# Optimization experiments

Measured on AMD Instinct MI355X. Metric: run time of the kernel, lower is better.

## Reference

```python
import jax, jax.numpy as jnp
import numpy as np

N = 50000      # nodes
E = 800000     # edges (avg degree 16)
IN_DIM = 64
EMB = 64
L = 4          # num_layer
BN_EPS = 1e-5


def setup_inputs() -> dict:
    key = jax.random.key(0)
    ks = jax.random.split(key, 8)
    s = 0.05
    return {
        "x": jax.random.normal(ks[0], (N, 1, IN_DIM), jnp.float32),
        "edge_index": jax.random.randint(ks[1], (2, E), 0, N, jnp.int32),
        "edge_attr": jax.random.normal(ks[2], (E, 3), jnp.float32),
        "edge_weight": jax.random.uniform(ks[3], (E,), jnp.float32),
        # atom encoder Linear(in_dim, emb)
        "ae_w": jax.random.normal(ks[4], (IN_DIM, EMB), jnp.float32) * s,
        "ae_b": jnp.zeros((EMB,), jnp.float32),
        # per-layer GIN MLP: Linear -> BN -> ReLU -> Linear (stacked over L)
        "W1": jax.random.normal(ks[5], (L, EMB, EMB), jnp.float32) * s,
        "b1": jnp.zeros((L, EMB), jnp.float32),
        "g1": jnp.ones((L, EMB), jnp.float32),
        "be1": jnp.zeros((L, EMB), jnp.float32),
        "W2": jax.random.normal(ks[6], (L, EMB, EMB), jnp.float32) * s,
        "b2": jnp.zeros((L, EMB), jnp.float32),
        # outer per-layer BatchNorm1d in GNN_node
        "g_out": jnp.ones((L, EMB), jnp.float32),
        "be_out": jnp.zeros((L, EMB), jnp.float32),
    }


def _bn(h, g, b):
    # BatchNorm1d, training mode: batch stats over node dim, biased variance
    m = h.mean(0)
    v = h.var(0)
    return (h - m) * jax.lax.rsqrt(v + BN_EPS) * g + b


def reference(x, edge_index, edge_attr, edge_weight,
              ae_w, ae_b, W1, b1, g1, be1, W2, b2, g_out, be_out):
    # atom encoder on x[:, 0] : [N, in_dim] -> [N, emb]
    h = x[:, 0] @ ae_w + ae_b
    src = edge_index[0]
    dst = edge_index[1]
    n = h.shape[0]
    num_layers = W1.shape[0]
    for l in range(num_layers):
        # MyPyGINConv (train_eps=False, eps=0): scatter-add of x_j * w_e, plus self term
        msg = h[src] * edge_weight[:, None]                      # [E, emb]
        agg = jax.ops.segment_sum(msg, dst, num_segments=n)      # [N, emb]
        out = agg + h                                            # (1+eps)*x_r, eps=0
        # conv MLP: Linear -> BN -> ReLU -> Linear
        out = jax.nn.relu(_bn(out @ W1[l] + b1[l], g1[l], be1[l]))
        out = out @ W2[l] + b2[l]
        # outer BN + ReLU (always applied for 'originalgin'); dropout p=0; residual
        out = jax.nn.relu(_bn(out, g_out[l], be_out[l]))
        h = out + h
    return h  # JK='last'
```

## Files before the change

### kernel.cpp

```cpp
#include <hip/hip_runtime.h>
#include <stdint.h>

#define EMB 64
#define BN_EPS 1e-5f
#define BSH 8
#define CHUNK 4096
#define TS 68
#define NHB 120

typedef short bfrag __attribute__((ext_vector_type(8)));
typedef float f32x4 __attribute__((ext_vector_type(4)));

#define IN_F32    0
#define IN_BF16   1
#define IN_BF16BN 2

__device__ __forceinline__ unsigned short f2b(float x) {
    unsigned u = __float_as_uint(x);
    u += 0x7FFFu + ((u >> 16) & 1u);
    return (unsigned short)(u >> 16);
}
__device__ __forceinline__ float b2f(unsigned short v) {
    return __uint_as_float(((unsigned)v) << 16);
}

__global__ void __launch_bounds__(256) k_prep_hist(
        const float* __restrict__ ae_w, const float* __restrict__ W1,
        const float* __restrict__ W2, unsigned short* __restrict__ Wt16,
        int* __restrict__ hist_part, float* __restrict__ stats,
        const int* __restrict__ ei, int E, int L, int nstats) {
    __shared__ int lh[256];
    const int tid = threadIdx.x;
    const int nw = (1 + 2 * L) * EMB * EMB;
    for (int gid = blockIdx.x * 256 + tid; gid < nw; gid += gridDim.x * 256) {
        int m = gid >> 12;
        int j = (gid >> 6) & 63;
        int k = gid & 63;
        const float* src = (m == 0) ? ae_w
                         : (m <= L ? W1 + (size_t)(m - 1) * EMB * EMB
                                   : W2 + (size_t)(m - 1 - L) * EMB * EMB);
        Wt16[gid] = f2b(src[k * EMB + j]);
    }
    for (int i = blockIdx.x * 256 + tid; i < nstats; i += gridDim.x * 256)
        stats[i] = 0.0f;
    if (blockIdx.x < NHB) {
        lh[tid] = 0;
        __syncthreads();
        for (int e = blockIdx.x * 256 + tid; e < E; e += NHB * 256)
            atomicAdd(&lh[((unsigned)ei[E + e]) >> BSH], 1);
        __syncthreads();
        hist_part[blockIdx.x * 256 + tid] = lh[tid];
    }
}

__global__ void __launch_bounds__(256) k_bscan(const int* __restrict__ hist_part,
                                               int* __restrict__ bbase,
                                               int* __restrict__ bcur, int nb) {
    __shared__ int a[256];
    const int t = threadIdx.x;
    int v = 0;
    for (int b = 0; b < NHB; b++) v += hist_part[b * 256 + t];
    a[t] = v;
    __syncthreads();
    for (int off = 1; off < 256; off <<= 1) {
        int x = (t >= off) ? a[t - off] : 0;
        __syncthreads();
        a[t] += x;
        __syncthreads();
    }
    int excl = a[t] - v;
    if (t < nb) { bbase[t] = excl; bcur[t] = excl; }
    if (t == nb - 1) bbase[nb] = a[t];
}

__global__ void __launch_bounds__(256) k_part(
        const int* __restrict__ ei, const float* __restrict__ ew,
        int* __restrict__ bcur, int2* __restrict__ eG, int E) {
    __shared__ int lcnt[256], lbase[256], loff[256];
    const int tid = threadIdx.x;
    const int c0 = blockIdx.x * CHUNK;
    lcnt[tid] = 0;
    __syncthreads();
    int src[16], pk[16], g[16];
    float wt[16];
#pragma unroll
    for (int i = 0; i < 16; i++) {
        int e = c0 + i * 256 + tid;
        if (e < E) {
            int d = ei[E + e];
            src[i] = ei[e];
            wt[i] = ew[e];
            g[i] = ((unsigned)d) >> BSH;
            pk[i] = src[i] | ((d & 255) << 24);
            atomicAdd(&lcnt[g[i]], 1);
        } else g[i] = -1;
    }
    __syncthreads();
    if (lcnt[tid]) lbase[tid] = atomicAdd(&bcur[tid], lcnt[tid]);
    loff[tid] = 0;
    __syncthreads();
#pragma unroll
    for (int i = 0; i < 16; i++) {
        if (g[i] >= 0) {
            int pos = lbase[g[i]] + atomicAdd(&loff[g[i]], 1);
            eG[pos] = make_int2(pk[i], __float_as_int(wt[i]));
        }
    }
}

__global__ void __launch_bounds__(256) k_build(
        const int2* __restrict__ eG, const int* __restrict__ bbase,
        int* __restrict__ rowst, int* __restrict__ counts,
        int2* __restrict__ pairs, int N) {
    __shared__ int lcnt[256], a[256], lcur[256];
    const int t = threadIdx.x;
    const int b = blockIdx.x;
    const int e0 = bbase[b], e1 = bbase[b + 1];
    lcnt[t] = 0;
    __syncthreads();
    for (int i = e0 + t; i < e1; i += 256)
        atomicAdd(&lcnt[((unsigned)eG[i].x) >> 24], 1);
    __syncthreads();
    int v = lcnt[t];
    a[t] = v;
    __syncthreads();
    for (int off = 1; off < 256; off <<= 1) {
        int x = (t >= off) ? a[t - off] : 0;
        __syncthreads();
        a[t] += x;
        __syncthreads();
    }
    int excl = a[t] - v;
    lcur[t] = excl;
    int node = (b << BSH) + t;
    if (node < N) { rowst[node] = e0 + excl; counts[node] = v; }
    __syncthreads();
    for (int i = e0 + t; i < e1; i += 256) {
        int2 p = eG[i];
        int loc = ((unsigned)p.x) >> 24;
        int pos = e0 + atomicAdd(&lcur[loc], 1);
        pairs[pos] = make_int2(p.x & 0x00FFFFFF, p.y);
    }
}

__global__ void k_agg(const unsigned short* __restrict__ hb,
                      const int* __restrict__ rowst,
                      const int* __restrict__ counts, const int2* __restrict__ pairs,
                      unsigned short* __restrict__ out16, int N) {
    const int lane = threadIdx.x & 63;
    int wave = (blockIdx.x * blockDim.x + threadIdx.x) >> 6;
    const int nwaves = (gridDim.x * blockDim.x) >> 6;
    for (int nA = wave; nA < N; nA += 2 * nwaves) {
        const int nB = nA + nwaves;
        const int uA = __builtin_amdgcn_readfirstlane(nA);
        const int uB = __builtin_amdgcn_readfirstlane(nB);
        const bool hasB = uB < N;
        int sA = rowst[uA], eA = sA + counts[uA];
        int sB = 0, eB = 0;
        if (hasB) { sB = rowst[uB]; eB = sB + counts[uB]; }
        float aA[8] = {0, 0, 0, 0, 0, 0, 0, 0};
        float aB[8] = {0, 0, 0, 0, 0, 0, 0, 0};
        for (int xA = sA, xB = sB; (xA < eA) | (xB < eB); xA += 8, xB += 8) {
            int2 pA[8], pB[8];
            float wA[8], wB[8];
#pragma unroll
            for (int k = 0; k < 8; k++) {
                int i = xA + k;
                bool ok = i < eA;
                int2 p = pairs[ok ? i : 0];
                pA[k] = p;
                wA[k] = ok ? __int_as_float(p.y) : 0.f;
            }
#pragma unroll
            for (int k = 0; k < 8; k++) {
                int i = xB + k;
                bool ok = i < eB;
                int2 p = pairs[ok ? i : 0];
                pB[k] = p;
                wB[k] = ok ? __int_as_float(p.y) : 0.f;
            }
#pragma unroll
            for (int k = 0; k < 8; k++)
                aA[k] = fmaf(wA[k], b2f(hb[(size_t)pA[k].x * EMB + lane]), aA[k]);
#pragma unroll
            for (int k = 0; k < 8; k++)
                aB[k] = fmaf(wB[k], b2f(hb[(size_t)pB[k].x * EMB + lane]), aB[k]);
        }
        float sumA = (((aA[0] + aA[1]) + (aA[2] + aA[3])) +
                      ((aA[4] + aA[5]) + (aA[6] + aA[7]))) +
                     b2f(hb[(size_t)uA * EMB + lane]);
        out16[(size_t)uA * EMB + lane] = f2b(sumA);
        if (hasB) {
            float sumB = (((aB[0] + aB[1]) + (aB[2] + aB[3])) +
                          ((aB[4] + aB[5]) + (aB[6] + aB[7]))) +
                         b2f(hb[(size_t)uB * EMB + lane]);
            out16[(size_t)uB * EMB + lane] = f2b(sumB);
        }
    }
}

template <int INMODE, bool DO_STATS>
__global__ void __launch_bounds__(256) k_mmx(
        const void* __restrict__ in_v, const unsigned short* __restrict__ Wt,
        const float* __restrict__ bias, const float* __restrict__ stats,
        const float* __restrict__ g, const float* __restrict__ be, float invN,
        unsigned short* __restrict__ out16, float* __restrict__ st_out, int N) {
    __shared__ float tb[64 * TS];
    __shared__ float st_part[128];
    __shared__ float scs[EMB], shs[EMB];
    const int tid = threadIdx.x;
    const int lane = tid & 63;
    const int wv = tid >> 6;
    const int node0 = blockIdx.x * 64;
    const int m = lane & 15;
    const int quad = lane >> 4;

    if (DO_STATS && tid < 128) st_part[tid] = 0.f;
    if (INMODE == IN_BF16BN) {
        if (tid < EMB) {
            float s1 = 0.f, s2 = 0.f;
#pragma unroll
            for (int k = 0; k < 8; k++) {
                s1 += stats[k * 128 + tid];
                s2 += stats[k * 128 + 64 + tid];
            }
            float mm = s1 * invN;
            float va = fmaf(s2, invN, -mm * mm);
            float rs = rsqrtf(va + BN_EPS);
            float sc = rs * g[tid];
            scs[tid] = sc;
            shs[tid] = fmaf(-mm, sc, be[tid]);
        }
        __syncthreads();
    }

    const int arow = node0 + wv * 16 + m;
    bfrag a0 = {0, 0, 0, 0, 0, 0, 0, 0}, a1 = {0, 0, 0, 0, 0, 0, 0, 0};
    if (arow < N) {
        if (INMODE == IN_BF16) {
            const unsigned short* ab =
                (const unsigned short*)in_v + (size_t)arow * EMB + quad * 8;
            a0 = *(const bfrag*)ab;
            a1 = *(const bfrag*)(ab + 32);
        } else if (INMODE == IN_BF16BN) {
            const unsigned short* ab =
                (const unsigned short*)in_v + (size_t)arow * EMB + quad * 8;
            bfrag r0 = *(const bfrag*)ab;
            bfrag r1 = *(const bfrag*)(ab + 32);
#pragma unroll
            for (int j = 0; j < 8; j++) {
                int k0 = quad * 8 + j;
                float v0 = b2f((unsigned short)r0[j]);
                float v1 = b2f((unsigned short)r1[j]);
                v0 = fmaxf(0.f, fmaf(v0, scs[k0], shs[k0]));
                v1 = fmaxf(0.f, fmaf(v1, scs[k0 + 32], shs[k0 + 32]));
                a0[j] = (short)f2b(v0);
                a1[j] = (short)f2b(v1);
            }
        } else {
            const float* af = (const float*)in_v + (size_t)arow * EMB + quad * 8;
#pragma unroll
            for (int j = 0; j < 8; j++) {
                a0[j] = (short)f2b(af[j]);
                a1[j] = (short)f2b(af[32 + j]);
            }
        }
    }

    const unsigned short* bb = Wt + (size_t)m * EMB + quad * 8;
    f32x4 acc[4];
#pragma unroll
    for (int c = 0; c < 4; c++) {
        bfrag b0 = *(const bfrag*)(bb + c * 16 * EMB);
        bfrag b1 = *(const bfrag*)(bb + c * 16 * EMB + 32);
        f32x4 z = {0.f, 0.f, 0.f, 0.f};
        z = __builtin_amdgcn_mfma_f32_16x16x32_bf16(a0, b0, z, 0, 0, 0);
        z = __builtin_amdgcn_mfma_f32_16x16x32_bf16(a1, b1, z, 0, 0, 0);
        acc[c] = z;
    }

#pragma unroll
    for (int c = 0; c < 4; c++) {
        float bj = bias[c * 16 + m];
#pragma unroll
        for (int r = 0; r < 4; r++) {
            int row = wv * 16 + quad * 4 + r;
            float v = (node0 + row < N) ? (acc[c][r] + bj) : 0.f;
            tb[row * TS + c * 16 + m] = v;
        }
    }
    __syncthreads();

    if (DO_STATS) {
        float ssum = 0.f, ssq = 0.f;
#pragma unroll
        for (int i = 0; i < 16; i++) {
            float v = tb[(wv * 16 + i) * TS + lane];
            ssum += v;
            ssq = fmaf(v, v, ssq);
        }
        atomicAdd(&st_part[lane], ssum);
        atomicAdd(&st_part[64 + lane], ssq);
    }

    ushort4* o4 = (ushort4*)(out16 + (size_t)node0 * EMB);
#pragma unroll
    for (int it = 0; it < 4; it++) {
        int flat4 = it * 256 + tid;
        int nsub = flat4 >> 4;
        int c4 = flat4 & 15;
        if (node0 + nsub < N) {
            const float* s4 = tb + nsub * TS + c4 * 4;
            ushort4 o;
            o.x = f2b(s4[0]); o.y = f2b(s4[1]);
            o.z = f2b(s4[2]); o.w = f2b(s4[3]);
            o4[flat4] = o;
        }
    }

    if (DO_STATS) {
        __syncthreads();
        if (tid < 128)
            atomicAdd(&st_out[((unsigned)blockIdx.x & 7u) * 128 + tid], st_part[tid]);
    }
}

template <bool LAST>
__global__ void k_bnres(const unsigned short* __restrict__ u16,
                        const float* __restrict__ st,
                        const float* __restrict__ g, const float* __restrict__ be,
                        unsigned short* __restrict__ hb16, float* __restrict__ out32,
                        float invN, int total4) {
    __shared__ float scs[EMB], shs[EMB];
    const int tid = threadIdx.x;
    if (tid < EMB) {
        float s1 = 0.f, s2 = 0.f;
#pragma unroll
        for (int k = 0; k < 8; k++) {
            s1 += st[k * 128 + tid];
            s2 += st[k * 128 + 64 + tid];
        }
        float mm = s1 * invN;
        float va = fmaf(s2, invN, -mm * mm);
        float rs = rsqrtf(va + BN_EPS);
        float sc = rs * g[tid];
        scs[tid] = sc;
        shs[tid] = fmaf(-mm, sc, be[tid]);
    }
    __syncthreads();
    int stride = gridDim.x * blockDim.x;
    for (int i4 = blockIdx.x * blockDim.x + tid; i4 < total4; i4 += stride) {
        int c4 = i4 & 15;
        ushort4 uv = ((const ushort4*)u16)[i4];
        ushort4 hv = ((const ushort4*)hb16)[i4];
        float4 scv = *(const float4*)&scs[c4 * 4];
        float4 shv = *(const float4*)&shs[c4 * 4];
        float4 o;
        o.x = fmaxf(0.f, fmaf(b2f(uv.x), scv.x, shv.x)) + b2f(hv.x);
        o.y = fmaxf(0.f, fmaf(b2f(uv.y), scv.y, shv.y)) + b2f(hv.y);
        o.z = fmaxf(0.f, fmaf(b2f(uv.z), scv.z, shv.z)) + b2f(hv.z);
        o.w = fmaxf(0.f, fmaf(b2f(uv.w), scv.w, shv.w)) + b2f(hv.w);
        if (LAST) {
            ((float4*)out32)[i4] = o;
        } else {
            ushort4 ob;
            ob.x = f2b(o.x); ob.y = f2b(o.y);
            ob.z = f2b(o.z); ob.w = f2b(o.w);
            ((ushort4*)hb16)[i4] = ob;
        }
    }
}

extern "C" void kernel_launch(void* const* d_in, const int* in_sizes, int n_in,
                              void* d_out, int out_size, void* d_ws, size_t ws_size,
                              hipStream_t stream) {
    const float* x     = (const float*)d_in[0];
    const int*   ei    = (const int*)d_in[1];
    const float* ew    = (const float*)d_in[3];
    const float* ae_w  = (const float*)d_in[4];
    const float* ae_b  = (const float*)d_in[5];
    const float* W1    = (const float*)d_in[6];
    const float* b1    = (const float*)d_in[7];
    const float* g1    = (const float*)d_in[8];
    const float* be1   = (const float*)d_in[9];
    const float* W2    = (const float*)d_in[10];
    const float* b2    = (const float*)d_in[11];
    const float* g_out = (const float*)d_in[12];
    const float* be_out= (const float*)d_in[13];

    const int N = in_sizes[0] / EMB;
    const int E = in_sizes[3];
    const int L = in_sizes[6] / (EMB * EMB);
    const float invN = 1.0f / (float)N;
    const int NBUCK = (N + 255) >> BSH;

    uintptr_t p = (uintptr_t)d_ws;
    auto alloc = [&](size_t bytes) -> void* {
        p = (p + 255) & ~(uintptr_t)255;
        void* r = (void*)p;
        p += bytes;
        return r;
    };
    unsigned short* hb16 = (unsigned short*)alloc((size_t)N * EMB * 2);
    unsigned short* b16a = (unsigned short*)alloc((size_t)N * EMB * 2);
    unsigned short* t16  = (unsigned short*)alloc((size_t)N * EMB * 2);
    unsigned short* Wt16 = (unsigned short*)alloc((size_t)(1 + 2 * L) * EMB * EMB * 2);
    int*   counts= (int*)alloc((size_t)N * 4);
    int*   rowst = (int*)alloc((size_t)N * 4);
    int*   hist_part = (int*)alloc((size_t)NHB * 256 * 4);
    int*   bbase = (int*)alloc(257 * 4);
    int*   bcur  = (int*)alloc(256 * 4);
    int2*  pairs = (int2*)alloc((size_t)E * 8);
    int2*  eG    = (int2*)alloc((size_t)E * 8);
    float* stats = (float*)alloc((size_t)L * 2 * 8 * 128 * 4);
    (void)ws_size; (void)n_in; (void)out_size;

    const int nw = (1 + 2 * L) * EMB * EMB;
    const int nstats = L * 2 * 8 * 128;
    const int nprep = (nw + 255) / 256;
    hipLaunchKernelGGL(k_prep_hist, dim3(nprep > NHB ? nprep : NHB), dim3(256), 0,
                       stream, ae_w, W1, W2, Wt16, hist_part, stats, ei, E, L, nstats);

    const int ntiles = (N + 63) / 64;
    hipLaunchKernelGGL((k_mmx<IN_F32, false>), dim3(ntiles), dim3(256), 0, stream,
                       x, Wt16, ae_b, (const float*)nullptr, (const float*)nullptr,
                       (const float*)nullptr, 0.f, hb16, (float*)nullptr, N);

    hipLaunchKernelGGL(k_bscan, dim3(1), dim3(256), 0, stream,
                       hist_part, bbase, bcur, NBUCK);
    hipLaunchKernelGGL(k_part, dim3((E + CHUNK - 1) / CHUNK), dim3(256), 0, stream,
                       ei, ew, bcur, eG, E);
    hipLaunchKernelGGL(k_build, dim3(NBUCK), dim3(256), 0, stream,
                       eG, bbase, rowst, counts, pairs, N);

    for (int l = 0; l < L; l++) {
        float* stats1 = stats + (size_t)(l * 2 + 0) * 1024;
        float* stats2 = stats + (size_t)(l * 2 + 1) * 1024;

        hipLaunchKernelGGL(k_agg, dim3(2048), dim3(256), 0, stream,
                           hb16, rowst, counts, pairs, b16a, N);
        hipLaunchKernelGGL((k_mmx<IN_BF16, true>), dim3(ntiles), dim3(256), 0, stream,
                           b16a, Wt16 + (size_t)(1 + l) * EMB * EMB, b1 + (size_t)l * EMB,
                           (const float*)nullptr, (const float*)nullptr,
                           (const float*)nullptr, 0.f, t16, stats1, N);
        hipLaunchKernelGGL((k_mmx<IN_BF16BN, true>), dim3(ntiles), dim3(256), 0, stream,
                           t16, Wt16 + (size_t)(1 + L + l) * EMB * EMB, b2 + (size_t)l * EMB,
                           stats1, g1 + (size_t)l * EMB, be1 + (size_t)l * EMB, invN,
                           b16a, stats2, N);
        if (l == L - 1) {
            hipLaunchKernelGGL((k_bnres<true>), dim3(1024), dim3(256), 0, stream,
                               b16a, stats2, g_out + (size_t)l * EMB,
                               be_out + (size_t)l * EMB, hb16, (float*)d_out,
                               invN, N * 16);
        } else {
            hipLaunchKernelGGL((k_bnres<false>), dim3(1024), dim3(256), 0, stream,
                               b16a, stats2, g_out + (size_t)l * EMB,
                               be_out + (size_t)l * EMB, hb16, (float*)nullptr,
                               invN, N * 16);
        }
    }
}
```

Baseline: 403.7 us.

## Fuse encoder with prep/histogram, merge bucket scan into partition, pair-edge aggregation

The atom-encoder GEMM is merged into the prep/histogram kernel, and that kernel now takes one histogram per edge chunk. The separate bucket-scan kernel is removed: each partition block computes its own prefix from the per-chunk histograms, which gives deterministic bucket offsets without global atomics. The aggregation kernel now has each half-wave process a different edge and load 32-bit pairs of bf16 features, then combines the halves with shuffles. This cuts launches and gather instructions, at the cost of every partition block redundantly re-reading all chunk histograms.

```diff
diff --git a/kernel.cpp b/kernel.cpp
--- a/kernel.cpp
+++ b/kernel.cpp
@@ -6,7 +6,7 @@
 #define BSH 8
 #define CHUNK 4096
 #define TS 68
-#define NHB 120
+#define ALS 72
 
 typedef short bfrag __attribute__((ext_vector_type(8)));
 typedef float f32x4 __attribute__((ext_vector_type(4)));
@@ -15,188 +15,274 @@
 #define IN_BF16   1
 #define IN_BF16BN 2
 
+struct SMM {
+  float tb[64 * TS];
+  float st[128];
+  float scs[EMB], shs[EMB];
+  unsigned short wb[4096];
+};
+
 __device__ __forceinline__ unsigned short f2b(float x) {
-    unsigned u = __float_as_uint(x);
-    u += 0x7FFFu + ((u >> 16) & 1u);
-    return (unsigned short)(u >> 16);
+  unsigned u = __float_as_uint(x);
+  u += 0x7FFFu + ((u >> 16) & 1u);
+  return (unsigned short)(u >> 16);
 }
 __device__ __forceinline__ float b2f(unsigned short v) {
-    return __uint_as_float(((unsigned)v) << 16);
-}
-
-__global__ void __launch_bounds__(256) k_prep_hist(
-        const float* __restrict__ ae_w, const float* __restrict__ W1,
-        const float* __restrict__ W2, unsigned short* __restrict__ Wt16,
-        int* __restrict__ hist_part, float* __restrict__ stats,
-        const int* __restrict__ ei, int E, int L, int nstats) {
-    __shared__ int lh[256];
-    const int tid = threadIdx.x;
-    const int nw = (1 + 2 * L) * EMB * EMB;
-    for (int gid = blockIdx.x * 256 + tid; gid < nw; gid += gridDim.x * 256) {
-        int m = gid >> 12;
-        int j = (gid >> 6) & 63;
-        int k = gid & 63;
-        const float* src = (m == 0) ? ae_w
-                         : (m <= L ? W1 + (size_t)(m - 1) * EMB * EMB
-                                   : W2 + (size_t)(m - 1 - L) * EMB * EMB);
-        Wt16[gid] = f2b(src[k * EMB + j]);
-    }
-    for (int i = blockIdx.x * 256 + tid; i < nstats; i += gridDim.x * 256)
-        stats[i] = 0.0f;
-    if (blockIdx.x < NHB) {
-        lh[tid] = 0;
-        __syncthreads();
-        for (int e = blockIdx.x * 256 + tid; e < E; e += NHB * 256)
-            atomicAdd(&lh[((unsigned)ei[E + e]) >> BSH], 1);
-        __syncthreads();
-        hist_part[blockIdx.x * 256 + tid] = lh[tid];
-    }
-}
-
-__global__ void __launch_bounds__(256) k_bscan(const int* __restrict__ hist_part,
-                                               int* __restrict__ bbase,
-                                               int* __restrict__ bcur, int nb) {
-    __shared__ int a[256];
-    const int t = threadIdx.x;
-    int v = 0;
-    for (int b = 0; b < NHB; b++) v += hist_part[b * 256 + t];
-    a[t] = v;
-    __syncthreads();
-    for (int off = 1; off < 256; off <<= 1) {
-        int x = (t >= off) ? a[t - off] : 0;
-        __syncthreads();
-        a[t] += x;
-        __syncthreads();
-    }
-    int excl = a[t] - v;
-    if (t < nb) { bbase[t] = excl; bcur[t] = excl; }
-    if (t == nb - 1) bbase[nb] = a[t];
+  return __uint_as_float(((unsigned)v) << 16);
+}
+
+__device__ __forceinline__ void enc_tile(SMM& sm, int tile,
+    const float* x, const float* aewf, const float* bias,
+    unsigned short* out16, int N) {
+  const int tid = threadIdx.x;
+  const int lane = tid & 63;
+  const int wv = tid >> 6;
+  const int r = wv >> 1;
+  const int c0 = (wv & 1) * 2;
+  const int m = lane & 15;
+  const int quad = lane >> 4;
+  const int node0 = tile * 64;
+
+#pragma unroll
+  for (int it = 0; it < 8; it++) {
+    int idx = it * 512 + tid;
+    int j = idx >> 6, k = idx & 63;
+    sm.wb[idx] = f2b(aewf[k * EMB + j]);
+  }
+  __syncthreads();
+
+  bfrag a0 = {0, 0, 0, 0, 0, 0, 0, 0}, a1 = {0, 0, 0, 0, 0, 0, 0, 0};
+  const int arow = node0 + r * 16 + m;
+  if (arow < N) {
+    const float* af = x + (size_t)arow * EMB + quad * 8;
+#pragma unroll
+    for (int j = 0; j < 8; j++) {
+      a0[j] = (short)f2b(af[j]);
+      a1[j] = (short)f2b(af[32 + j]);
+    }
+  }
+  f32x4 zz[2];
+#pragma unroll
+  for (int cc = 0; cc < 2; cc++) {
+    const int c = c0 + cc;
+    const unsigned short* bb = &sm.wb[(c * 16 + m) * EMB + quad * 8];
+    bfrag b0 = *(const bfrag*)bb;
+    bfrag b1 = *(const bfrag*)(bb + 32);
+    f32x4 z = {0.f, 0.f, 0.f, 0.f};
+    z = __builtin_amdgcn_mfma_f32_16x16x32_bf16(a0, b0, z, 0, 0, 0);
+    z = __builtin_amdgcn_mfma_f32_16x16x32_bf16(a1, b1, z, 0, 0, 0);
+    zz[cc] = z;
+  }
+#pragma unroll
+  for (int cc = 0; cc < 2; cc++) {
+    const int c = c0 + cc;
+    float bj = bias[c * 16 + m];
+#pragma unroll
+    for (int reg = 0; reg < 4; reg++) {
+      int row = r * 16 + quad * 4 + reg;
+      float v = (node0 + row < N) ? (zz[cc][reg] + bj) : 0.f;
+      sm.tb[row * TS + c * 16 + m] = v;
+    }
+  }
+  __syncthreads();
+  ushort4* o4 = (ushort4*)(out16 + (size_t)node0 * EMB);
+#pragma unroll
+  for (int it = 0; it < 2; it++) {
+    int flat4 = it * 512 + tid;
+    int nsub = flat4 >> 4;
+    int c4 = flat4 & 15;
+    if (node0 + nsub < N) {
+      const float* s4 = sm.tb + nsub * TS + c4 * 4;
+      ushort4 o;
+      o.x = f2b(s4[0]); o.y = f2b(s4[1]);
+      o.z = f2b(s4[2]); o.w = f2b(s4[3]);
+      o4[flat4] = o;
+    }
+  }
+}
+
+__global__ void __launch_bounds__(512) k_enc_prep(
+        const float* __restrict__ x, const float* __restrict__ ae_w,
+        const float* __restrict__ ae_b,
+        const float* __restrict__ W1, const float* __restrict__ W2,
+        unsigned short* __restrict__ Wt16, int* __restrict__ hist_part,
+        float* __restrict__ stats, const int* __restrict__ ei,
+        unsigned short* __restrict__ hb16,
+        int E, int L, int nstats, int ntiles, int nchunks, int N) {
+  __shared__ SMM sm;
+  if ((int)blockIdx.x < ntiles) {
+    enc_tile(sm, blockIdx.x, x, ae_w, ae_b, hb16, N);
+    return;
+  }
+  const int pb = blockIdx.x - ntiles;
+  const int tid = threadIdx.x;
+  int* lh = (int*)sm.tb;
+  const int nw2 = 2 * L * EMB * EMB;
+  for (int gid = pb * 512 + tid; gid < nw2; gid += nchunks * 512) {
+    int mI = gid >> 12;
+    int j = (gid >> 6) & 63;
+    int k = gid & 63;
+    const float* src = (mI < L) ? W1 + (size_t)mI * EMB * EMB
+                                : W2 + (size_t)(mI - L) * EMB * EMB;
+    Wt16[EMB * EMB + gid] = f2b(src[k * EMB + j]);
+  }
+  for (int i = pb * 512 + tid; i < nstats; i += nchunks * 512) stats[i] = 0.0f;
+  if (tid < 256) lh[tid] = 0;
+  __syncthreads();
+  const int c0 = pb * CHUNK;
+  const int cend = min(c0 + CHUNK, E);
+  for (int e = c0 + tid; e < cend; e += 512)
+    atomicAdd(&lh[((unsigned)ei[E + e]) >> BSH], 1);
+  __syncthreads();
+  if (tid < 256) hist_part[pb * 256 + tid] = lh[tid];
 }
 
 __global__ void __launch_bounds__(256) k_part(
         const int* __restrict__ ei, const float* __restrict__ ew,
-        int* __restrict__ bcur, int2* __restrict__ eG, int E) {
-    __shared__ int lcnt[256], lbase[256], loff[256];
-    const int tid = threadIdx.x;
-    const int c0 = blockIdx.x * CHUNK;
-    lcnt[tid] = 0;
+        const int* __restrict__ hist_part, int* __restrict__ bbase,
+        int2* __restrict__ eG, int E, int nchunks, int nb) {
+  __shared__ int a[256], lbase[256], loff[256];
+  const int t = threadIdx.x;
+  const int c = blockIdx.x;
+  int pre = 0, tot = 0;
+  for (int cc = 0; cc < nchunks; cc++) {
+    int v = hist_part[cc * 256 + t];
+    pre += (cc < c) ? v : 0;
+    tot += v;
+  }
+  a[t] = tot;
+  __syncthreads();
+  for (int off = 1; off < 256; off <<= 1) {
+    int x = (t >= off) ? a[t - off] : 0;
     __syncthreads();
-    int src[16], pk[16], g[16];
-    float wt[16];
-#pragma unroll
-    for (int i = 0; i < 16; i++) {
-        int e = c0 + i * 256 + tid;
-        if (e < E) {
-            int d = ei[E + e];
-            src[i] = ei[e];
-            wt[i] = ew[e];
-            g[i] = ((unsigned)d) >> BSH;
-            pk[i] = src[i] | ((d & 255) << 24);
-            atomicAdd(&lcnt[g[i]], 1);
-        } else g[i] = -1;
-    }
+    a[t] += x;
     __syncthreads();
-    if (lcnt[tid]) lbase[tid] = atomicAdd(&bcur[tid], lcnt[tid]);
-    loff[tid] = 0;
-    __syncthreads();
-#pragma unroll
-    for (int i = 0; i < 16; i++) {
-        if (g[i] >= 0) {
-            int pos = lbase[g[i]] + atomicAdd(&loff[g[i]], 1);
-            eG[pos] = make_int2(pk[i], __float_as_int(wt[i]));
-        }
-    }
+  }
+  int excl = a[t] - tot;
+  lbase[t] = excl + pre;
+  loff[t] = 0;
+  if (c == 0 && t <= nb) bbase[t] = excl;
+  __syncthreads();
+  const int c0 = c * CHUNK;
+#pragma unroll 4
+  for (int i = 0; i < 16; i++) {
+    int e = c0 + i * 256 + t;
+    if (e < E) {
+      int d = ei[E + e];
+      int g = ((unsigned)d) >> BSH;
+      int pk = ei[e] | ((d & 255) << 24);
+      int pos = lbase[g] + atomicAdd(&loff[g], 1);
+      eG[pos] = make_int2(pk, __float_as_int(ew[e]));
+    }
+  }
 }
 
 __global__ void __launch_bounds__(256) k_build(
         const int2* __restrict__ eG, const int* __restrict__ bbase,
         int* __restrict__ rowst, int* __restrict__ counts,
         int2* __restrict__ pairs, int N) {
-    __shared__ int lcnt[256], a[256], lcur[256];
-    const int t = threadIdx.x;
-    const int b = blockIdx.x;
-    const int e0 = bbase[b], e1 = bbase[b + 1];
-    lcnt[t] = 0;
+  __shared__ int lcnt[256], a[256], lcur[256];
+  const int t = threadIdx.x;
+  const int b = blockIdx.x;
+  const int e0 = bbase[b], e1 = bbase[b + 1];
+  lcnt[t] = 0;
+  __syncthreads();
+  for (int i = e0 + t; i < e1; i += 256)
+    atomicAdd(&lcnt[((unsigned)eG[i].x) >> 24], 1);
+  __syncthreads();
+  int v = lcnt[t];
+  a[t] = v;
+  __syncthreads();
+  for (int off = 1; off < 256; off <<= 1) {
+    int x = (t >= off) ? a[t - off] : 0;
     __syncthreads();
-    for (int i = e0 + t; i < e1; i += 256)
-        atomicAdd(&lcnt[((unsigned)eG[i].x) >> 24], 1);
+    a[t] += x;
     __syncthreads();
-    int v = lcnt[t];
-    a[t] = v;
-    __syncthreads();
-    for (int off = 1; off < 256; off <<= 1) {
-        int x = (t >= off) ? a[t - off] : 0;
-        __syncthreads();
-        a[t] += x;
-        __syncthreads();
-    }
-    int excl = a[t] - v;
-    lcur[t] = excl;
-    int node = (b << BSH) + t;
-    if (node < N) { rowst[node] = e0 + excl; counts[node] = v; }
-    __syncthreads();
-    for (int i = e0 + t; i < e1; i += 256) {
-        int2 p = eG[i];
-        int loc = ((unsigned)p.x) >> 24;
-        int pos = e0 + atomicAdd(&lcur[loc], 1);
-        pairs[pos] = make_int2(p.x & 0x00FFFFFF, p.y);
-    }
+  }
+  int excl = a[t] - v;
+  lcur[t] = excl;
+  int node = (b << BSH) + t;
+  if (node < N) { rowst[node] = e0 + excl; counts[node] = v; }
+  __syncthreads();
+  for (int i = e0 + t; i < e1; i += 256) {
+    int2 p = eG[i];
+    int loc = ((unsigned)p.x) >> 24;
+    int pos = e0 + atomicAdd(&lcur[loc], 1);
+    pairs[pos] = make_int2(p.x & 0x00FFFFFF, p.y);
+  }
 }
 
 __global__ void k_agg(const unsigned short* __restrict__ hb,
                       const int* __restrict__ rowst,
                       const int* __restrict__ counts, const int2* __restrict__ pairs,
                       unsigned short* __restrict__ out16, int N) {
-    const int lane = threadIdx.x & 63;
-    int wave = (blockIdx.x * blockDim.x + threadIdx.x) >> 6;
-    const int nwaves = (gridDim.x * blockDim.x) >> 6;
-    for (int nA = wave; nA < N; nA += 2 * nwaves) {
-        const int nB = nA + nwaves;
-        const int uA = __builtin_amdgcn_readfirstlane(nA);
-        const int uB = __builtin_amdgcn_readfirstlane(nB);
-        const bool hasB = uB < N;
-        int sA = rowst[uA], eA = sA + counts[uA];
-        int sB = 0, eB = 0;
-        if (hasB) { sB = rowst[uB]; eB = sB + counts[uB]; }
-        float aA[8] = {0, 0, 0, 0, 0, 0, 0, 0};
-        float aB[8] = {0, 0, 0, 0, 0, 0, 0, 0};
-        for (int xA = sA, xB = sB; (xA < eA) | (xB < eB); xA += 8, xB += 8) {
-            int2 pA[8], pB[8];
-            float wA[8], wB[8];
-#pragma unroll
-            for (int k = 0; k < 8; k++) {
-                int i = xA + k;
-                bool ok = i < eA;
-                int2 p = pairs[ok ? i : 0];
-                pA[k] = p;
-                wA[k] = ok ? __int_as_float(p.y) : 0.f;
-            }
-#pragma unroll
-            for (int k = 0; k < 8; k++) {
-                int i = xB + k;
-                bool ok = i < eB;
-                int2 p = pairs[ok ? i : 0];
-                pB[k] = p;
-                wB[k] = ok ? __int_as_float(p.y) : 0.f;
-            }
-#pragma unroll
-            for (int k = 0; k < 8; k++)
-                aA[k] = fmaf(wA[k], b2f(hb[(size_t)pA[k].x * EMB + lane]), aA[k]);
-#pragma unroll
-            for (int k = 0; k < 8; k++)
-                aB[k] = fmaf(wB[k], b2f(hb[(size_t)pB[k].x * EMB + lane]), aB[k]);
-        }
-        float sumA = (((aA[0] + aA[1]) + (aA[2] + aA[3])) +
-                      ((aA[4] + aA[5]) + (aA[6] + aA[7]))) +
-                     b2f(hb[(size_t)uA * EMB + lane]);
-        out16[(size_t)uA * EMB + lane] = f2b(sumA);
-        if (hasB) {
-            float sumB = (((aB[0] + aB[1]) + (aB[2] + aB[3])) +
-                          ((aB[4] + aB[5]) + (aB[6] + aB[7]))) +
-                         b2f(hb[(size_t)uB * EMB + lane]);
-            out16[(size_t)uB * EMB + lane] = f2b(sumB);
-        }
-    }
+  const int lane = threadIdx.x & 63;
+  const int half = lane >> 5;
+  const int col = lane & 31;
+  int wave = (blockIdx.x * blockDim.x + threadIdx.x) >> 6;
+  const int nwaves = (gridDim.x * blockDim.x) >> 6;
+  for (int nA = wave; nA < N; nA += 2 * nwaves) {
+    const int nB = nA + nwaves;
+    const int uA = __builtin_amdgcn_readfirstlane(nA);
+    const int uB = __builtin_amdgcn_readfirstlane(nB);
+    const bool hasB = uB < N;
+    int sA = rowst[uA], eA = sA + counts[uA];
+    int sB = 0, eB = 0;
+    if (hasB) { sB = rowst[uB]; eB = sB + counts[uB]; }
+    float a0A[4] = {0, 0, 0, 0}, a1A[4] = {0, 0, 0, 0};
+    float a0B[4] = {0, 0, 0, 0}, a1B[4] = {0, 0, 0, 0};
+    for (int xA = sA, xB = sB; (xA < eA) | (xB < eB); xA += 8, xB += 8) {
+      int2 pA[8], pB[8];
+#pragma unroll
+      for (int k = 0; k < 8; k++) {
+        int ia = xA + k;
+        pA[k] = pairs[ia < eA ? ia : 0];
+      }
+#pragma unroll
+      for (int k = 0; k < 8; k++) {
+        int ib = xB + k;
+        pB[k] = pairs[ib < eB ? ib : 0];
+      }
+#pragma unroll
+      for (int j = 0; j < 4; j++) {
+        int2 pp = half ? pA[2 * j + 1] : pA[2 * j];
+        bool ok = (xA + 2 * j + half) < eA;
+        float w = ok ? __int_as_float(pp.y) : 0.f;
+        unsigned v = *((const unsigned*)(hb + (size_t)pp.x * EMB) + col);
+        a0A[j] = fmaf(w, b2f((unsigned short)(v & 0xFFFFu)), a0A[j]);
+        a1A[j] = fmaf(w, b2f((unsigned short)(v >> 16)), a1A[j]);
+      }
+#pragma unroll
+      for (int j = 0; j < 4; j++) {
+        int2 pp = half ? pB[2 * j + 1] : pB[2 * j];
+        bool ok = (xB + 2 * j + half) < eB;
+        float w = ok ? __int_as_float(pp.y) : 0.f;
+        unsigned v = *((const unsigned*)(hb + (size_t)pp.x * EMB) + col);
+        a0B[j] = fmaf(w, b2f((unsigned short)(v & 0xFFFFu)), a0B[j]);
+        a1B[j] = fmaf(w, b2f((unsigned short)(v >> 16)), a1B[j]);
+      }
+    }
+    {
+      float s0 = (a0A[0] + a0A[1]) + (a0A[2] + a0A[3]);
+      float s1 = (a1A[0] + a1A[1]) + (a1A[2] + a1A[3]);
+      s0 += __shfl_xor(s0, 32);
+      s1 += __shfl_xor(s1, 32);
+      float v0 = __shfl(s0, lane >> 1);
+      float v1 = __shfl(s1, lane >> 1);
+      float sum = ((lane & 1) ? v1 : v0) + b2f(hb[(size_t)uA * EMB + lane]);
+      out16[(size_t)uA * EMB + lane] = f2b(sum);
+    }
+    if (hasB) {
+      float s0 = (a0B[0] + a0B[1]) + (a0B[2] + a0B[3]);
+      float s1 = (a1B[0] + a1B[1]) + (a1B[2] + a1B[3]);
+      s0 += __shfl_xor(s0, 32);
+      s1 += __shfl_xor(s1, 32);
+      float v0 = __shfl(s0, lane >> 1);
+      float v1 = __shfl(s1, lane >> 1);
+      float sum = ((lane & 1) ? v1 : v0) + b2f(hb[(size_t)uB * EMB + lane]);
+      out16[(size_t)uB * EMB + lane] = f2b(sum);
+    }
+  }
 }
 
 template <int INMODE, bool DO_STATS>
@@ -205,124 +291,117 @@
         const float* __restrict__ bias, const float* __restrict__ stats,
         const float* __restrict__ g, const float* __restrict__ be, float invN,
         unsigned short* __restrict__ out16, float* __restrict__ st_out, int N) {
-    __shared__ float tb[64 * TS];
-    __shared__ float st_part[128];
-    __shared__ float scs[EMB], shs[EMB];
-    const int tid = threadIdx.x;
-    const int lane = tid & 63;
-    const int wv = tid >> 6;
-    const int node0 = blockIdx.x * 64;
-    const int m = lane & 15;
-    const int quad = lane >> 4;
-
-    if (DO_STATS && tid < 128) st_part[tid] = 0.f;
-    if (INMODE == IN_BF16BN) {
-        if (tid < EMB) {
-            float s1 = 0.f, s2 = 0.f;
-#pragma unroll
-            for (int k = 0; k < 8; k++) {
-                s1 += stats[k * 128 + tid];
-                s2 += stats[k * 128 + 64 + tid];
-            }
-            float mm = s1 * invN;
-            float va = fmaf(s2, invN, -mm * mm);
-            float rs = rsqrtf(va + BN_EPS);
-            float sc = rs * g[tid];
-            scs[tid] = sc;
-            shs[tid] = fmaf(-mm, sc, be[tid]);
-        }
-        __syncthreads();
-    }
-
-    const int arow = node0 + wv * 16 + m;
-    bfrag a0 = {0, 0, 0, 0, 0, 0, 0, 0}, a1 = {0, 0, 0, 0, 0, 0, 0, 0};
-    if (arow < N) {
-        if (INMODE == IN_BF16) {
-            const unsigned short* ab =
-                (const unsigned short*)in_v + (size_t)arow * EMB + quad * 8;
-            a0 = *(const bfrag*)ab;
-            a1 = *(const bfrag*)(ab + 32);
-        } else if (INMODE == IN_BF16BN) {
-            const unsigned short* ab =
-                (const unsigned short*)in_v + (size_t)arow * EMB + quad * 8;
-            bfrag r0 = *(const bfrag*)ab;
-            bfrag r1 = *(const bfrag*)(ab + 32);
-#pragma unroll
-            for (int j = 0; j < 8; j++) {
-                int k0 = quad * 8 + j;
-                float v0 = b2f((unsigned short)r0[j]);
-                float v1 = b2f((unsigned short)r1[j]);
-                v0 = fmaxf(0.f, fmaf(v0, scs[k0], shs[k0]));
-                v1 = fmaxf(0.f, fmaf(v1, scs[k0 + 32], shs[k0 + 32]));
-                a0[j] = (short)f2b(v0);
-                a1[j] = (short)f2b(v1);
-            }
-        } else {
-            const float* af = (const float*)in_v + (size_t)arow * EMB + quad * 8;
-#pragma unroll
-            for (int j = 0; j < 8; j++) {
-                a0[j] = (short)f2b(af[j]);
-                a1[j] = (short)f2b(af[32 + j]);
-            }
-        }
-    }
-
-    const unsigned short* bb = Wt + (size_t)m * EMB + quad * 8;
-    f32x4 acc[4];
-#pragma unroll
-    for (int c = 0; c < 4; c++) {
-        bfrag b0 = *(const bfrag*)(bb + c * 16 * EMB);
-        bfrag b1 = *(const bfrag*)(bb + c * 16 * EMB + 32);
-        f32x4 z = {0.f, 0.f, 0.f, 0.f};
-        z = __builtin_amdgcn_mfma_f32_16x16x32_bf16(a0, b0, z, 0, 0, 0);
-        z = __builtin_amdgcn_mfma_f32_16x16x32_bf16(a1, b1, z, 0, 0, 0);
-        acc[c] = z;
-    }
-
-#pragma unroll
-    for (int c = 0; c < 4; c++) {
-        float bj = bias[c * 16 + m];
-#pragma unroll
-        for (int r = 0; r < 4; r++) {
-            int row = wv * 16 + quad * 4 + r;
-            float v = (node0 + row < N) ? (acc[c][r] + bj) : 0.f;
-            tb[row * TS + c * 16 + m] = v;
-        }
+  __shared__ float tb[64 * TS];
+  __shared__ float st_part[128];
+  __shared__ float scs[EMB], shs[EMB];
+  const int tid = threadIdx.x;
+  const int lane = tid & 63;
+  const int wv = tid >> 6;
+  const int node0 = blockIdx.x * 64;
+  const int m = lane & 15;
+  const int quad = lane >> 4;
+
+  if (DO_STATS && tid < 128) st_part[tid] = 0.f;
+  if (INMODE == IN_BF16BN) {
+    if (tid < EMB) {
+      float s1 = 0.f, s2 = 0.f;
+#pragma unroll
+      for (int k = 0; k < 8; k++) {
+        s1 += stats[k * 128 + tid];
+        s2 += stats[k * 128 + 64 + tid];
+      }
+      float mm = s1 * invN;
+      float va = fmaf(s2, invN, -mm * mm);
+      float rs = rsqrtf(va + BN_EPS);
+      float sc = rs * g[tid];
+      scs[tid] = sc;
+      shs[tid] = fmaf(-mm, sc, be[tid]);
     }
     __syncthreads();
-
-    if (DO_STATS) {
-        float ssum = 0.f, ssq = 0.f;
-#pragma unroll
-        for (int i = 0; i < 16; i++) {
-            float v = tb[(wv * 16 + i) * TS + lane];
-            ssum += v;
-            ssq = fmaf(v, v, ssq);
-        }
-        atomicAdd(&st_part[lane], ssum);
-        atomicAdd(&st_part[64 + lane], ssq);
-    }
-
-    ushort4* o4 = (ushort4*)(out16 + (size_t)node0 * EMB);
-#pragma unroll
-    for (int it = 0; it < 4; it++) {
-        int flat4 = it * 256 + tid;
-        int nsub = flat4 >> 4;
-        int c4 = flat4 & 15;
-        if (node0 + nsub < N) {
-            const float* s4 = tb + nsub * TS + c4 * 4;
-            ushort4 o;
-            o.x = f2b(s4[0]); o.y = f2b(s4[1]);
-            o.z = f2b(s4[2]); o.w = f2b(s4[3]);
-            o4[flat4] = o;
-        }
-    }
-
-    if (DO_STATS) {
-        __syncthreads();
-        if (tid < 128)
-            atomicAdd(&st_out[((unsigned)blockIdx.x & 7u) * 128 + tid], st_part[tid]);
-    }
+  }
+
+  const int arow = node0 + wv * 16 + m;
+  bfrag a0 = {0, 0, 0, 0, 0, 0, 0, 0}, a1 = {0, 0, 0, 0, 0, 0, 0, 0};
+  if (arow < N) {
+    if (INMODE == IN_BF16) {
+      const unsigned short* ab =
+          (const unsigned short*)in_v + (size_t)arow * EMB + quad * 8;
+      a0 = *(const bfrag*)ab;
+      a1 = *(const bfrag*)(ab + 32);
+    } else if (INMODE == IN_BF16BN) {
+      const unsigned short* ab =
+          (const unsigned short*)in_v + (size_t)arow * EMB + quad * 8;
+      bfrag r0 = *(const bfrag*)ab;
+      bfrag r1 = *(const bfrag*)(ab + 32);
+#pragma unroll
+      for (int j = 0; j < 8; j++) {
+        int k0 = quad * 8 + j;
+        float v0 = b2f((unsigned short)r0[j]);
+        float v1 = b2f((unsigned short)r1[j]);
+        v0 = fmaxf(0.f, fmaf(v0, scs[k0], shs[k0]));
+        v1 = fmaxf(0.f, fmaf(v1, scs[k0 + 32], shs[k0 + 32]));
+        a0[j] = (short)f2b(v0);
+        a1[j] = (short)f2b(v1);
+      }
+    }
+  }
+
+  const unsigned short* bb = Wt + (size_t)m * EMB + quad * 8;
+  f32x4 acc[4];
+#pragma unroll
+  for (int c = 0; c < 4; c++) {
+    bfrag b0 = *(const bfrag*)(bb + c * 16 * EMB);
+    bfrag b1 = *(const bfrag*)(bb + c * 16 * EMB + 32);
+    f32x4 z = {0.f, 0.f, 0.f, 0.f};
+    z = __builtin_amdgcn_mfma_f32_16x16x32_bf16(a0, b0, z, 0, 0, 0);
+    z = __builtin_amdgcn_mfma_f32_16x16x32_bf16(a1, b1, z, 0, 0, 0);
+    acc[c] = z;
+  }
+
+#pragma unroll
+  for (int c = 0; c < 4; c++) {
+    float bj = bias[c * 16 + m];
+#pragma unroll
+    for (int r = 0; r < 4; r++) {
+      int row = wv * 16 + quad * 4 + r;
+      float v = (node0 + row < N) ? (acc[c][r] + bj) : 0.f;
+      tb[row * TS + c * 16 + m] = v;
+    }
+  }
+  __syncthreads();
+
+  if (DO_STATS) {
+    float ssum = 0.f, ssq = 0.f;
+#pragma unroll
+    for (int i = 0; i < 16; i++) {
+      float v = tb[(wv * 16 + i) * TS + lane];
+      ssum += v;
+      ssq = fmaf(v, v, ssq);
+    }
+    atomicAdd(&st_part[lane], ssum);
+    atomicAdd(&st_part[64 + lane], ssq);
+  }
+
+  ushort4* o4 = (ushort4*)(out16 + (size_t)node0 * EMB);
+#pragma unroll
+  for (int it = 0; it < 4; it++) {
+    int flat4 = it * 256 + tid;
+    int nsub = flat4 >> 4;
+    int c4 = flat4 & 15;
+    if (node0 + nsub < N) {
+      const float* s4 = tb + nsub * TS + c4 * 4;
+      ushort4 o;
+      o.x = f2b(s4[0]); o.y = f2b(s4[1]);
+      o.z = f2b(s4[2]); o.w = f2b(s4[3]);
+      o4[flat4] = o;
+    }
+  }
+
+  if (DO_STATS) {
+    __syncthreads();
+    if (tid < 128)
+      atomicAdd(&st_out[((unsigned)blockIdx.x & 7u) * 128 + tid], st_part[tid]);
+  }
 }
 
 template <bool LAST>
@@ -331,132 +410,125 @@
                         const float* __restrict__ g, const float* __restrict__ be,
                         unsigned short* __restrict__ hb16, float* __restrict__ out32,
                         float invN, int total4) {
-    __shared__ float scs[EMB], shs[EMB];
-    const int tid = threadIdx.x;
-    if (tid < EMB) {
-        float s1 = 0.f, s2 = 0.f;
-#pragma unroll
-        for (int k = 0; k < 8; k++) {
-            s1 += st[k * 128 + tid];
-            s2 += st[k * 128 + 64 + tid];
-        }
-        float mm = s1 * invN;
-        float va = fmaf(s2, invN, -mm * mm);
-        float rs = rsqrtf(va + BN_EPS);
-        float sc = rs * g[tid];
-        scs[tid] = sc;
-        shs[tid] = fmaf(-mm, sc, be[tid]);
-    }
-    __syncthreads();
-    int stride = gridDim.x * blockDim.x;
-    for (int i4 = blockIdx.x * blockDim.x + tid; i4 < total4; i4 += stride) {
-        int c4 = i4 & 15;
-        ushort4 uv = ((const ushort4*)u16)[i4];
-        ushort4 hv = ((const ushort4*)hb16)[i4];
-        float4 scv = *(const float4*)&scs[c4 * 4];
-        float4 shv = *(const float4*)&shs[c4 * 4];
-        float4 o;
-        o.x = fmaxf(0.f, fmaf(b2f(uv.x), scv.x, shv.x)) + b2f(hv.x);
-        o.y = fmaxf(0.f, fmaf(b2f(uv.y), scv.y, shv.y)) + b2f(hv.y);
-        o.z = fmaxf(0.f, fmaf(b2f(uv.z), scv.z, shv.z)) + b2f(hv.z);
-        o.w = fmaxf(0.f, fmaf(b2f(uv.w), scv.w, shv.w)) + b2f(hv.w);
-        if (LAST) {
-            ((float4*)out32)[i4] = o;
-        } else {
-            ushort4 ob;
-            ob.x = f2b(o.x); ob.y = f2b(o.y);
-            ob.z = f2b(o.z); ob.w = f2b(o.w);
-            ((ushort4*)hb16)[i4] = ob;
-        }
-    }
+  __shared__ float scs[EMB], shs[EMB];
+  const int tid = threadIdx.x;
+  if (tid < EMB) {
+    float s1 = 0.f, s2 = 0.f;
+#pragma unroll
+    for (int k = 0; k < 8; k++) {
+      s1 += st[k * 128 + tid];
+      s2 += st[k * 128 + 64 + tid];
+    }
+    float mm = s1 * invN;
+    float va = fmaf(s2, invN, -mm * mm);
+    float rs = rsqrtf(va + BN_EPS);
+    float sc = rs * g[tid];
+    scs[tid] = sc;
+    shs[tid] = fmaf(-mm, sc, be[tid]);
+  }
+  __syncthreads();
+  int stride = gridDim.x * blockDim.x;
+  for (int i4 = blockIdx.x * blockDim.x + tid; i4 < total4; i4 += stride) {
+    int c4 = i4 & 15;
+    ushort4 uv = ((const ushort4*)u16)[i4];
+    ushort4 hv = ((const ushort4*)hb16)[i4];
+    float4 scv = *(const float4*)&scs[c4 * 4];
+    float4 shv = *(const float4*)&shs[c4 * 4];
+    float4 o;
+    o.x = fmaxf(0.f, fmaf(b2f(uv.x), scv.x, shv.x)) + b2f(hv.x);
+    o.y = fmaxf(0.f, fmaf(b2f(uv.y), scv.y, shv.y)) + b2f(hv.y);
+    o.z = fmaxf(0.f, fmaf(b2f(uv.z), scv.z, shv.z)) + b2f(hv.z);
+    o.w = fmaxf(0.f, fmaf(b2f(uv.w), scv.w, shv.w)) + b2f(hv.w);
+    if (LAST) {
+      ((float4*)out32)[i4] = o;
+    } else {
+      ushort4 ob;
+      ob.x = f2b(o.x); ob.y = f2b(o.y);
+      ob.z = f2b(o.z); ob.w = f2b(o.w);
+      ((ushort4*)hb16)[i4] = ob;
+    }
+  }
 }
 
 extern "C" void kernel_launch(void* const* d_in, const int* in_sizes, int n_in,
                               void* d_out, int out_size, void* d_ws, size_t ws_size,
                               hipStream_t stream) {
-    const float* x     = (const float*)d_in[0];
-    const int*   ei    = (const int*)d_in[1];
-    const float* ew    = (const float*)d_in[3];
-    const float* ae_w  = (const float*)d_in[4];
-    const float* ae_b  = (const float*)d_in[5];
-    const float* W1    = (const float*)d_in[6];
-    const float* b1    = (const float*)d_in[7];
-    const float* g1    = (const float*)d_in[8];
-    const float* be1   = (const float*)d_in[9];
-    const float* W2    = (const float*)d_in[10];
-    const float* b2    = (const float*)d_in[11];
-    const float* g_out = (const float*)d_in[12];
-    const float* be_out= (const float*)d_in[13];
-
-    const int N = in_sizes[0] / EMB;
-    const int E = in_sizes[3];
-    const int L = in_sizes[6] / (EMB * EMB);
-    const float invN = 1.0f / (float)N;
-    const int NBUCK = (N + 255) >> BSH;
-
-    uintptr_t p = (uintptr_t)d_ws;
-    auto alloc = [&](size_t bytes) -> void* {
-        p = (p + 255) & ~(uintptr_t)255;
-        void* r = (void*)p;
-        p += bytes;
-        return r;
-    };
-    unsigned short* hb16 = (unsigned short*)alloc((size_t)N * EMB * 2);
-    unsigned short* b16a = (unsigned short*)alloc((size_t)N * EMB * 2);
-    unsigned short* t16  = (unsigned short*)alloc((size_t)N * EMB * 2);
-    unsigned short* Wt16 = (unsigned short*)alloc((size_t)(1 + 2 * L) * EMB * EMB * 2);
-    int*   counts= (int*)alloc((size_t)N * 4);
-    int*   rowst = (int*)alloc((size_t)N * 4);
-    int*   hist_part = (int*)alloc((size_t)NHB * 256 * 4);
-    int*   bbase = (int*)alloc(257 * 4);
-    int*   bcur  = (int*)alloc(256 * 4);
-    int2*  pairs = (int2*)alloc((size_t)E * 8);
-    int2*  eG    = (int2*)alloc((size_t)E * 8);
-    float* stats = (float*)alloc((size_t)L * 2 * 8 * 128 * 4);
-    (void)ws_size; (void)n_in; (void)out_size;
-
-    const int nw = (1 + 2 * L) * EMB * EMB;
-    const int nstats = L * 2 * 8 * 128;
-    const int nprep = (nw + 255) / 256;
-    hipLaunchKernelGGL(k_prep_hist, dim3(nprep > NHB ? nprep : NHB), dim3(256), 0,
-                       stream, ae_w, W1, W2, Wt16, hist_part, stats, ei, E, L, nstats);
-
-    const int ntiles = (N + 63) / 64;
-    hipLaunchKernelGGL((k_mmx<IN_F32, false>), dim3(ntiles), dim3(256), 0, stream,
-                       x, Wt16, ae_b, (const float*)nullptr, (const float*)nullptr,
-                       (const float*)nullptr, 0.f, hb16, (float*)nullptr, N);
-
-    hipLaunchKernelGGL(k_bscan, dim3(1), dim3(256), 0, stream,
-                       hist_part, bbase, bcur, NBUCK);
-    hipLaunchKernelGGL(k_part, dim3((E + CHUNK - 1) / CHUNK), dim3(256), 0, stream,
-                       ei, ew, bcur, eG, E);
-    hipLaunchKernelGGL(k_build, dim3(NBUCK), dim3(256), 0, stream,
-                       eG, bbase, rowst, counts, pairs, N);
-
-    for (int l = 0; l < L; l++) {
-        float* stats1 = stats + (size_t)(l * 2 + 0) * 1024;
-        float* stats2 = stats + (size_t)(l * 2 + 1) * 1024;
-
-        hipLaunchKernelGGL(k_agg, dim3(2048), dim3(256), 0, stream,
-                           hb16, rowst, counts, pairs, b16a, N);
-        hipLaunchKernelGGL((k_mmx<IN_BF16, true>), dim3(ntiles), dim3(256), 0, stream,
-                           b16a, Wt16 + (size_t)(1 + l) * EMB * EMB, b1 + (size_t)l * EMB,
-                           (const float*)nullptr, (const float*)nullptr,
-                           (const float*)nullptr, 0.f, t16, stats1, N);
-        hipLaunchKernelGGL((k_mmx<IN_BF16BN, true>), dim3(ntiles), dim3(256), 0, stream,
-                           t16, Wt16 + (size_t)(1 + L + l) * EMB * EMB, b2 + (size_t)l * EMB,
-                           stats1, g1 + (size_t)l * EMB, be1 + (size_t)l * EMB, invN,
-                           b16a, stats2, N);
-        if (l == L - 1) {
-            hipLaunchKernelGGL((k_bnres<true>), dim3(1024), dim3(256), 0, stream,
-                               b16a, stats2, g_out + (size_t)l * EMB,
-                               be_out + (size_t)l * EMB, hb16, (float*)d_out,
-                               invN, N * 16);
-        } else {
-            hipLaunchKernelGGL((k_bnres<false>), dim3(1024), dim3(256), 0, stream,
-                               b16a, stats2, g_out + (size_t)l * EMB,
-                               be_out + (size_t)l * EMB, hb16, (float*)nullptr,
-                               invN, N * 16);
-        }
-    }
-}
+  const float* x     = (const float*)d_in[0];
+  const int*   ei    = (const int*)d_in[1];
+  const float* ew    = (const float*)d_in[3];
+  const float* ae_w  = (const float*)d_in[4];
+  const float* ae_b  = (const float*)d_in[5];
+  const float* W1    = (const float*)d_in[6];
+  const float* b1    = (const float*)d_in[7];
+  const float* g1    = (const float*)d_in[8];
+  const float* be1   = (const float*)d_in[9];
+  const float* W2    = (const float*)d_in[10];
+  const float* b2    = (const float*)d_in[11];
+  const float* g_out = (const float*)d_in[12];
+  const float* be_out= (const float*)d_in[13];
+
+  const int N = in_sizes[0] / EMB;
+  const int E = in_sizes[3];
+  const int L = in_sizes[6] / (EMB * EMB);
+  const float invN = 1.0f / (float)N;
+  const int NBUCK = (N + 255) >> BSH;
+  const int nchunks = (E + CHUNK - 1) / CHUNK;
+
+  uintptr_t p = (uintptr_t)d_ws;
+  auto alloc = [&](size_t bytes) -> void* {
+    p = (p + 255) & ~(uintptr_t)255;
+    void* r = (void*)p;
+    p += bytes;
+    return r;
+  };
+  unsigned short* hb16 = (unsigned short*)alloc((size_t)N * EMB * 2);
+  unsigned short* b16a = (unsigned short*)alloc((size_t)N * EMB * 2);
+  unsigned short* t16  = (unsigned short*)alloc((size_t)N * EMB * 2);
+  unsigned short* Wt16 = (unsigned short*)alloc((size_t)(1 + 2 * L) * EMB * EMB * 2);
+  int*   counts= (int*)alloc((size_t)N * 4);
+  int*   rowst = (int*)alloc((size_t)N * 4);
+  int*   hist_part = (int*)alloc((size_t)nchunks * 256 * 4);
+  int*   bbase = (int*)alloc(257 * 4);
+  int2*  pairs = (int2*)alloc((size_t)E * 8);
+  int2*  eG    = (int2*)alloc((size_t)E * 8);
+  float* stats = (float*)alloc((size_t)L * 2 * 8 * 128 * 4);
+  (void)ws_size; (void)n_in; (void)out_size;
+
+  const int ntiles = (N + 63) / 64;
+  const int nstats = L * 2 * 8 * 128;
+
+  hipLaunchKernelGGL(k_enc_prep, dim3(ntiles + nchunks), dim3(512), 0, stream,
+                     x, ae_w, ae_b, W1, W2, Wt16, hist_part, stats, ei,
+                     hb16, E, L, nstats, ntiles, nchunks, N);
+  hipLaunchKernelGGL(k_part, dim3(nchunks), dim3(256), 0, stream,
+                     ei, ew, hist_part, bbase, eG, E, nchunks, NBUCK);
+  hipLaunchKernelGGL(k_build, dim3(NBUCK), dim3(256), 0, stream,
+                     eG, bbase, rowst, counts, pairs, N);
+
+  for (int l = 0; l < L; l++) {
+    float* stats1 = stats + (size_t)(l * 2 + 0) * 1024;
+    float* stats2 = stats + (size_t)(l * 2 + 1) * 1024;
+
+    hipLaunchKernelGGL(k_agg, dim3(2048), dim3(256), 0, stream,
+                       hb16, rowst, counts, pairs, b16a, N);
+    hipLaunchKernelGGL((k_mmx<IN_BF16, true>), dim3(ntiles), dim3(256), 0, stream,
+                       b16a, Wt16 + (size_t)(1 + l) * EMB * EMB, b1 + (size_t)l * EMB,
+                       (const float*)nullptr, (const float*)nullptr,
+                       (const float*)nullptr, 0.f, t16, stats1, N);
+    hipLaunchKernelGGL((k_mmx<IN_BF16BN, true>), dim3(ntiles), dim3(256), 0, stream,
+                       t16, Wt16 + (size_t)(1 + L + l) * EMB * EMB, b2 + (size_t)l * EMB,
+                       stats1, g1 + (size_t)l * EMB, be1 + (size_t)l * EMB, invN,
+                       b16a, stats2, N);
+    if (l == L - 1) {
+      hipLaunchKernelGGL((k_bnres<true>), dim3(1024), dim3(256), 0, stream,
+                         b16a, stats2, g_out + (size_t)l * EMB,
+                         be_out + (size_t)l * EMB, hb16, (float*)d_out,
+                         invN, N * 16);
+    } else {
+      hipLaunchKernelGGL((k_bnres<false>), dim3(1024), dim3(256), 0, stream,
+                         b16a, stats2, g_out + (size_t)l * EMB,
+                         be_out + (size_t)l * EMB, hb16, (float*)nullptr,
+                         invN, N * 16);
+    }
+  }
+}
```

After: 386.2 us. 4.3% less time.
